# Optimization experiments

Measured on AMD Instinct MI355X. Metric: run time of the kernel, lower is better.

The kernel has to match this reference:

```python
import jax, jax.numpy as jnp
import numpy as np

D_OUT = 1536
BN_EPS = 1e-5


def _batchnorm(h, g, b):
    # torch BatchNorm1d in training mode: biased batch stats
    m = jnp.mean(h, axis=0)
    v = jnp.var(h, axis=0)
    return g * (h - m) * jax.lax.rsqrt(v + BN_EPS) + b


def setup_inputs() -> dict:
    key = jax.random.key(0)
    ks = jax.random.split(key, 16)
    B = 8192
    d0, d1, dib = 1024, 768, 1024
    s = lambda d: (2.0 / d) ** 0.5
    inp = {
        "x0": jax.random.normal(ks[0], (B, d0), jnp.float32),
        "x1": jax.random.normal(ks[1], (B, d1), jnp.float32),
        "x_ib": jax.random.normal(ks[2], (B, dib), jnp.float32),
        # 7 expert projections per source (Reaction_Head_mini modeled as linear proj)
        "pW0": jax.random.normal(ks[3], (7, d0, D_OUT), jnp.float32) * s(d0),
        "pb0": jnp.zeros((7, D_OUT), jnp.float32),
        "pW1": jax.random.normal(ks[4], (7, d1, D_OUT), jnp.float32) * s(d1),
        "pb1": jnp.zeros((7, D_OUT), jnp.float32),
        "pWib": jax.random.normal(ks[5], (7, dib, D_OUT), jnp.float32) * s(dib),
        "pbib": jnp.zeros((7, D_OUT), jnp.float32),
        # MOE_Router_Sig: Linear(1024,512)+BN+relu -> Linear(512,100)+BN+tanh -> Linear(100,3)
        "rw1": jax.random.normal(ks[6], (d0, 512), jnp.float32) * s(d0),
        "rb1": jnp.zeros((512,), jnp.float32),
        "rg1": jnp.ones((512,), jnp.float32),
        "rbt1": jnp.zeros((512,), jnp.float32),
        "rw2": jax.random.normal(ks[7], (512, 100), jnp.float32) * s(512),
        "rb2": jnp.zeros((100,), jnp.float32),
        "rg2": jnp.ones((100,), jnp.float32),
        "rbt2": jnp.zeros((100,), jnp.float32),
        "rw3": jax.random.normal(ks[8], (100, 3), jnp.float32) * s(100),
        "rb3": jnp.zeros((3,), jnp.float32),
    }
    return inp


def reference(x0, x1, x_ib, pW0, pb0, pW1, pb1, pWib, pbib,
              rw1, rb1, rg1, rbt1, rw2, rb2, rg2, rbt2, rw3, rb3):
    # ---- expert projections (torch.no_grad in original) ----
    e0 = jnp.einsum('bd,kdf->bkf', x0, pW0) + pb0      # [B,7,1536]
    e1 = jnp.einsum('bd,kdf->bkf', x1, pW1) + pb1      # [B,7,1536]
    eib = jnp.einsum('bd,kdf->bkf', x_ib, pWib) + pbib # [B,7,1536]
    ex = jnp.concatenate([e0, e1, eib], axis=1)        # [B,21,1536]
    B = ex.shape[0]
    # seg_mean with segment length 7 -> [B,3,1536]
    ex = ex.reshape(B, 3, 7, D_OUT).mean(axis=2)
    ex = jax.lax.stop_gradient(ex)
    # ---- router: MOE_Router_Sig(x0) -> sigmoid -> softmax ----
    h = _batchnorm(x0 @ rw1 + rb1, rg1, rbt1)
    h = jax.nn.relu(h)
    h = _batchnorm(h @ rw2 + rb2, rg2, rbt2)
    h = jnp.tanh(h)
    logits = jax.nn.sigmoid(h @ rw3 + rb3)             # [B,3]
    w = jax.nn.softmax(logits, axis=-1)                # [B,3]
    # ---- weighted combine + L2 normalize ----
    out = jnp.sum(ex * w[:, :, None], axis=1)          # [B,1536]
    out = out / jnp.linalg.norm(out, axis=-1, keepdims=True).clip(1e-12)
    return out
```

## Files before the change

kernel.cpp:

```cpp
#include <hip/hip_runtime.h>
#include <stdint.h>

typedef __attribute__((ext_vector_type(8))) short short8;
typedef __attribute__((ext_vector_type(4))) float floatx4;

__device__ inline unsigned short f2bf(float f) {
    unsigned int u = __float_as_uint(f);
    u += 0x7fffu + ((u >> 16) & 1u);
    return (unsigned short)(u >> 16);
}

__device__ void avg_transpose_tile(const float* __restrict__ src,
                                   unsigned short* __restrict__ dst,
                                   int E, int K, int Nsrc, int Ndst, int ldb,
                                   float scale, int tile_x, int tile_y) {
    __shared__ float tile[32][33];
    const int tid = threadIdx.x;
    const int tx = tid & 31;
    const int ty = tid >> 5;
    const int kb = tile_x * 32;
    const int nb = tile_y * 32;
#pragma unroll
    for (int p = 0; p < 4; ++p) {
        int kl = ty + p * 8;
        int k = kb + kl;
        int n = nb + tx;
        float s = 0.f;
        if (k < K && n < Nsrc) {
            for (int e = 0; e < E; ++e)
                s += src[(size_t)e * K * Nsrc + (size_t)k * Nsrc + n];
        }
        tile[kl][tx] = s * scale;
    }
    __syncthreads();
#pragma unroll
    for (int p = 0; p < 4; ++p) {
        int nl = ty + p * 8;
        int n = nb + nl;
        int k = kb + tx;
        if (n < Ndst && k < K)
            dst[(size_t)n * ldb + k] = f2bf(tile[tx][nl]);
    }
}

__global__ __launch_bounds__(256) void prep(
    const float* __restrict__ pW0, const float* __restrict__ pW1,
    const float* __restrict__ pWib, const float* __restrict__ rw1,
    const float* __restrict__ rw2, const float* __restrict__ pb0,
    const float* __restrict__ pb1, const float* __restrict__ pbib,
    const float* __restrict__ x0,
    unsigned short* __restrict__ Wmt, unsigned short* __restrict__ rw1t,
    unsigned short* __restrict__ rw2t, float* __restrict__ bm0,
    float* __restrict__ bm1, float* __restrict__ bm2,
    float* __restrict__ stats_zero, unsigned short* __restrict__ X0b) {
    int id = blockIdx.x;
    int tid = threadIdx.x;
    if (id < 1536) {
        avg_transpose_tile(pW0, Wmt + 0, 7, 1024, 1536, 1536, 2816, 1.f / 7.f,
                           id % 32, id / 32);
    } else if (id < 2688) {
        int t = id - 1536;
        avg_transpose_tile(pW1, Wmt + 1024, 7, 768, 1536, 1536, 2816, 1.f / 7.f,
                           t % 24, t / 24);
    } else if (id < 4224) {
        int t = id - 2688;
        avg_transpose_tile(pWib, Wmt + 1792, 7, 1024, 1536, 1536, 2816,
                           1.f / 7.f, t % 32, t / 32);
    } else if (id < 4736) {
        int t = id - 4224;
        avg_transpose_tile(rw1, rw1t, 1, 1024, 512, 512, 1024, 1.f, t % 32,
                           t / 32);
    } else if (id < 4800) {
        int t = id - 4736;
        avg_transpose_tile(rw2, rw2t, 1, 512, 100, 128, 512, 1.f, t % 16,
                           t / 16);
    } else if (id < 4806) {
        int i = (id - 4800) * 256 + tid;
        if (i < 1536) {
            float s0 = 0.f, s1 = 0.f, s2 = 0.f;
            for (int e = 0; e < 7; ++e) {
                s0 += pb0[e * 1536 + i];
                s1 += pb1[e * 1536 + i];
                s2 += pbib[e * 1536 + i];
            }
            const float inv = 1.f / 7.f;
            bm0[i] = s0 * inv; bm1[i] = s1 * inv; bm2[i] = s2 * inv;
        }
    } else if (id < 4807) {
        for (int i = tid; i < 1280; i += 256) stats_zero[i] = 0.f;
    } else {
        int base = (id - 4807) * 1024;
#pragma unroll
        for (int k = 0; k < 4; ++k) {
            int i = base + k * 256 + tid;
            float4 v = ((const float4*)x0)[i];
            ushort4 o;
            o.x = f2bf(v.x); o.y = f2bf(v.y); o.z = f2bf(v.z); o.w = f2bf(v.w);
            ((ushort4*)X0b)[i] = o;
        }
    }
}

template <int MODE>
__global__ __launch_bounds__(256) void gemm_bt(
    const unsigned short* __restrict__ A, const unsigned short* __restrict__ Bt,
    float* __restrict__ C, int K, int Nreal, int ldc,
    const float* __restrict__ bias, float* __restrict__ sum,
    float* __restrict__ sumsq) {
    __shared__ __align__(16) unsigned short As[128 * 32];
    __shared__ __align__(16) unsigned short Bs[128 * 32];
    const int tid = threadIdx.x;
    const int lane = tid & 63;
    const int wv = tid >> 6;
    const int bm_off = blockIdx.x * 128;
    const int bn_off = blockIdx.y * 128;
    const int wm = (wv & 1) * 64;
    const int wn = (wv >> 1) * 64;
    floatx4 acc[4][4];
#pragma unroll
    for (int i = 0; i < 4; ++i)
#pragma unroll
        for (int j = 0; j < 4; ++j) acc[i][j] = (floatx4){0.f, 0.f, 0.f, 0.f};

    const int quad = lane >> 4;
    const int lrow = lane & 15;
    const int srow = lane >> 2;
    const int scol = (lane & 3) * 8;

    const unsigned short* Ag = A + (size_t)bm_off * K;
    const unsigned short* Bg = Bt + (size_t)bn_off * K;

    for (int k0 = 0; k0 < K; k0 += 32) {
#pragma unroll
        for (int r = 0; r < 2; ++r) {
            int chunk = r * 4 + wv;
            {
                const unsigned short* gp =
                    Ag + (size_t)(chunk * 16 + srow) * K + (k0 + scol);
                __builtin_amdgcn_global_load_lds(
                    (const __attribute__((address_space(1))) void*)gp,
                    (__attribute__((address_space(3))) void*)(As + chunk * 512),
                    16, 0, 0);
            }
            {
                const unsigned short* gp =
                    Bg + (size_t)(chunk * 16 + srow) * K + (k0 + scol);
                __builtin_amdgcn_global_load_lds(
                    (const __attribute__((address_space(1))) void*)gp,
                    (__attribute__((address_space(3))) void*)(Bs + chunk * 512),
                    16, 0, 0);
            }
        }
        __syncthreads();
        short8 af[4], bfr[4];
#pragma unroll
        for (int i = 0; i < 4; ++i)
            af[i] = *(const short8*)(As + (wm + i * 16 + lrow) * 32 + quad * 8);
#pragma unroll
        for (int j = 0; j < 4; ++j)
            bfr[j] = *(const short8*)(Bs + (wn + j * 16 + lrow) * 32 + quad * 8);
#pragma unroll
        for (int i = 0; i < 4; ++i)
#pragma unroll
            for (int j = 0; j < 4; ++j)
                acc[i][j] = __builtin_amdgcn_mfma_f32_16x16x32_bf16(
                    af[i], bfr[j], acc[i][j], 0, 0, 0);
        __syncthreads();
    }

    {
#pragma unroll
        for (int j = 0; j < 4; ++j) {
            int n = bn_off + wn + j * 16 + lrow;
            bool nok = (n < Nreal);
            float bv = nok ? bias[n] : 0.f;
            float s = 0.f, ss = 0.f;
#pragma unroll
            for (int i = 0; i < 4; ++i) {
#pragma unroll
                for (int r = 0; r < 4; ++r) {
                    float v = acc[i][j][r] + bv;
                    int m = bm_off + wm + i * 16 + quad * 4 + r;
                    if (nok) C[(size_t)m * ldc + n] = v;
                    s += v; ss += v * v;
                }
            }
            s += __shfl_xor(s, 16); s += __shfl_xor(s, 32);
            ss += __shfl_xor(ss, 16); ss += __shfl_xor(ss, 32);
            if (quad == 0 && nok) {
                atomicAdd(&sum[n], s);
                atomicAdd(&sumsq[n], ss);
            }
        }
    }
}

__global__ __launch_bounds__(512, 2) void gemm256(
    const unsigned short* __restrict__ A0, const unsigned short* __restrict__ A1,
    const unsigned short* __restrict__ A2, const unsigned short* __restrict__ Bt,
    float* __restrict__ C, int ldc,
    const float* __restrict__ w0, const float* __restrict__ w1,
    const float* __restrict__ w2, const float* __restrict__ g0,
    const float* __restrict__ g1, const float* __restrict__ g2) {
    __shared__ __align__(16) unsigned short lds[57344];
    unsigned short* Asb = lds;
    unsigned short* Bsb = lds + 32768;

    const int tid = threadIdx.x;
    const int lane = tid & 63;
    const int wv = tid >> 6;
    const int wm = wv >> 2;
    const int wn = wv & 3;
    const int quad = lane >> 4;
    const int lrow = lane & 15;

    int b = blockIdx.y * 32 + blockIdx.x;
    const int xcd = b & 7;
    const int loc = b >> 3;
    const int row0 = (xcd * 4 + (loc & 3)) * 256;
    const int col0 = (loc >> 2) * 192;

    const int rA = tid >> 2;
    const int slA = (tid & 3) ^ ((rA >> 1) & 3);
    const size_t sA0 = (size_t)(row0 + rA) * 1024 + slA * 8;
    const size_t sA1 = (size_t)(row0 + rA) * 768 + slA * 8;

    size_t srcB16;
    {
        int r = tid >> 2;
        int sl = (tid & 3) ^ ((r >> 1) & 3);
        srcB16 = (size_t)(col0 + r) * 2816 + sl * 8;
    }
    size_t srcB4[2];
#pragma unroll
    for (int d = 0; d < 2; ++d) {
        int byteoff = d * 2048 + tid * 4;
        int r = 128 + (byteoff >> 6);
        int sl = ((byteoff >> 4) & 3) ^ ((r >> 1) & 3);
        srcB4[d] = (size_t)(col0 + r) * 2816 + sl * 8 + ((tid & 3) << 1);
    }

    auto stageA = [&](int kt, int buf) {
        unsigned short* d0 = Asb + buf * 8192 + wv * 512;
        if (kt < 32) {
            const unsigned short* g = A0 + (size_t)kt * 32;
            __builtin_amdgcn_global_load_lds(
                (const __attribute__((address_space(1))) void*)(g + sA0),
                (__attribute__((address_space(3))) void*)d0, 16, 0, 0);
            __builtin_amdgcn_global_load_lds(
                (const __attribute__((address_space(1))) void*)(g + sA0 + 128 * 1024),
                (__attribute__((address_space(3))) void*)(d0 + 4096), 16, 0, 0);
        } else if (kt < 56) {
            const unsigned short* g = A1 + (size_t)(kt - 32) * 32;
            __builtin_amdgcn_global_load_lds(
                (const __attribute__((address_space(1))) void*)(g + sA1),
                (__attribute__((address_space(3))) void*)d0, 16, 0, 0);
            __builtin_amdgcn_global_load_lds(
                (const __attribute__((address_space(1))) void*)(g + sA1 + 128 * 768),
                (__attribute__((address_space(3))) void*)(d0 + 4096), 16, 0, 0);
        } else {
            const unsigned short* g = A2 + (size_t)(kt - 56) * 32;
            __builtin_amdgcn_global_load_lds(
                (const __attribute__((address_space(1))) void*)(g + sA0),
                (__attribute__((address_space(3))) void*)d0, 16, 0, 0);
            __builtin_amdgcn_global_load_lds(
                (const __attribute__((address_space(1))) void*)(g + sA0 + 128 * 1024),
                (__attribute__((address_space(3))) void*)(d0 + 4096), 16, 0, 0);
        }
    };
    auto stageB = [&](int kt, int buf) {
        const size_t k0 = (size_t)kt * 32;
        __builtin_amdgcn_global_load_lds(
            (const __attribute__((address_space(1))) void*)(Bt + srcB16 + k0),
            (__attribute__((address_space(3))) void*)(Bsb + buf * 6144 +
                                                     wv * 512),
            16, 0, 0);
#pragma unroll
        for (int d = 0; d < 2; ++d) {
            __builtin_amdgcn_global_load_lds(
                (const __attribute__((address_space(1))) void*)(Bt + srcB4[d] + k0),
                (__attribute__((address_space(3))) void*)(Bsb + buf * 6144 +
                                                         4096 + d * 1024 +
                                                         wv * 128),
                4, 0, 0);
        }
    };

    floatx4 acc[8][3];
#pragma unroll
    for (int i = 0; i < 8; ++i)
#pragma unroll
        for (int j = 0; j < 3; ++j) acc[i][j] = (floatx4){0.f, 0.f, 0.f, 0.f};

    const int NT = 88;
    stageA(0, 0); stageB(0, 0);
    stageA(1, 1); stageB(1, 1);
    stageA(2, 2); stageB(2, 2);
    asm volatile("s_waitcnt vmcnt(10)" ::: "memory");
    asm volatile("s_barrier" ::: "memory");

    for (int t = 0; t < NT; ++t) {
        const int buf = t & 3;
        const int nb = (t + 3) & 3;
        const bool pre = (t + 3 < NT);
        const unsigned short* Ab = Asb + buf * 8192;
        const unsigned short* Bb = Bsb + buf * 6144;

        if (pre) stageA(t + 3, nb);
        short8 bfr[3];
#pragma unroll
        for (int j = 0; j < 3; ++j) {
            int r = wn * 48 + j * 16 + lrow;
            bfr[j] = *(const short8*)(Bb + r * 32 +
                                      ((quad ^ ((r >> 1) & 3)) << 3));
        }
        short8 af0[4];
#pragma unroll
        for (int i = 0; i < 4; ++i) {
            int r = wm * 128 + i * 16 + lrow;
            af0[i] = *(const short8*)(Ab + r * 32 +
                                      ((quad ^ ((r >> 1) & 3)) << 3));
        }
        __builtin_amdgcn_s_setprio(1);
#pragma unroll
        for (int i = 0; i < 4; ++i)
#pragma unroll
            for (int j = 0; j < 3; ++j)
                acc[i][j] = __builtin_amdgcn_mfma_f32_16x16x32_bf16(
                    af0[i], bfr[j], acc[i][j], 0, 0, 0);
        __builtin_amdgcn_s_setprio(0);

        if (pre) stageB(t + 3, nb);
        short8 af1[4];
#pragma unroll
        for (int i = 0; i < 4; ++i) {
            int r = wm * 128 + 64 + i * 16 + lrow;
            af1[i] = *(const short8*)(Ab + r * 32 +
                                      ((quad ^ ((r >> 1) & 3)) << 3));
        }
        __builtin_amdgcn_s_setprio(1);
#pragma unroll
        for (int i = 0; i < 4; ++i)
#pragma unroll
            for (int j = 0; j < 3; ++j)
                acc[4 + i][j] = __builtin_amdgcn_mfma_f32_16x16x32_bf16(
                    af1[i], bfr[j], acc[4 + i][j], 0, 0, 0);
        __builtin_amdgcn_s_setprio(0);

        if (t == 31) {
#pragma unroll
            for (int ii = 0; ii < 8; ++ii) {
#pragma unroll
                for (int r = 0; r < 4; ++r) {
                    float f = w0[row0 + wm * 128 + ii * 16 + quad * 4 + r];
#pragma unroll
                    for (int j = 0; j < 3; ++j) acc[ii][j][r] *= f;
                }
            }
        }

        if (t + 1 < NT) {
            if (t + 3 < NT)
                asm volatile("s_waitcnt vmcnt(10)" ::: "memory");
            else if (t + 2 < NT)
                asm volatile("s_waitcnt vmcnt(5)" ::: "memory");
            else
                asm volatile("s_waitcnt vmcnt(0)" ::: "memory");
            asm volatile("s_barrier" ::: "memory");
        }
    }

#pragma unroll
    for (int ii = 0; ii < 8; ++ii) {
#pragma unroll
        for (int r = 0; r < 4; ++r) {
            int m = row0 + wm * 128 + ii * 16 + quad * 4 + r;
            float a0 = w0[m], a1 = w1[m], a2 = w2[m];
#pragma unroll
            for (int j = 0; j < 3; ++j) {
                int n = col0 + wn * 48 + j * 16 + lrow;
                C[(size_t)m * ldc + n] =
                    acc[ii][j][r] + a0 * g0[n] + a1 * g1[n] + a2 * g2[n];
            }
        }
    }
}

__global__ __launch_bounds__(256) void bn_relu_pack(
    const float* __restrict__ h, unsigned short* __restrict__ out,
    const float* __restrict__ sum, const float* __restrict__ sumsq,
    const float* __restrict__ g, const float* __restrict__ b) {
    __shared__ float sc[512], sh[512];
    const float invB = 1.f / 8192.f;
    for (int c = threadIdx.x; c < 512; c += 256) {
        float m = sum[c] * invB;
        float v = sumsq[c] * invB - m * m;
        float s = g[c] * rsqrtf(v + 1e-5f);
        sc[c] = s;
        sh[c] = b[c] - m * s;
    }
    __syncthreads();
    int base = blockIdx.x * 4096;
#pragma unroll
    for (int k = 0; k < 16; ++k) {
        int i = base + k * 256 + threadIdx.x;
        int c4 = (i & 127) * 4;
        float4 v = ((const float4*)h)[i];
        ushort4 o;
        o.x = f2bf(fmaxf(v.x * sc[c4 + 0] + sh[c4 + 0], 0.f));
        o.y = f2bf(fmaxf(v.y * sc[c4 + 1] + sh[c4 + 1], 0.f));
        o.z = f2bf(fmaxf(v.z * sc[c4 + 2] + sh[c4 + 2], 0.f));
        o.w = f2bf(fmaxf(v.w * sc[c4 + 3] + sh[c4 + 3], 0.f));
        ((ushort4*)out)[i] = o;
    }
}

__global__ __launch_bounds__(128) void router_tail(
    const float* __restrict__ h2, const float* __restrict__ sum,
    const float* __restrict__ sumsq, const float* __restrict__ g,
    const float* __restrict__ b, const float* __restrict__ rw3,
    const float* __restrict__ rb3, float* __restrict__ w0,
    float* __restrict__ w1, float* __restrict__ w2) {
    __shared__ float sc[100], sh[100], w3[300], b3[3];
    int tid = threadIdx.x;
    const float invB = 1.f / 8192.f;
    if (tid < 100) {
        float m = sum[tid] * invB;
        float v = sumsq[tid] * invB - m * m;
        float s = g[tid] * rsqrtf(v + 1e-5f);
        sc[tid] = s;
        sh[tid] = b[tid] - m * s;
    }
    for (int i = tid; i < 300; i += 128) w3[i] = rw3[i];
    if (tid < 3) b3[tid] = rb3[tid];
    __syncthreads();
    int bi = blockIdx.x * 128 + tid;
    float l0 = b3[0], l1 = b3[1], l2 = b3[2];
    const float* hr = h2 + (size_t)bi * 100;
    for (int k = 0; k < 100; ++k) {
        float t = tanhf(hr[k] * sc[k] + sh[k]);
        l0 += t * w3[k * 3 + 0];
        l1 += t * w3[k * 3 + 1];
        l2 += t * w3[k * 3 + 2];
    }
    l0 = 1.f / (1.f + expf(-l0));
    l1 = 1.f / (1.f + expf(-l1));
    l2 = 1.f / (1.f + expf(-l2));
    float mx = fmaxf(l0, fmaxf(l1, l2));
    float e0 = expf(l0 - mx), e1 = expf(l1 - mx), e2 = expf(l2 - mx);
    float inv = 1.f / (e0 + e1 + e2);
    w0[bi] = e0 * inv; w1[bi] = e1 * inv; w2[bi] = e2 * inv;
}

__global__ __launch_bounds__(256) void pack1ib(
    const float* __restrict__ x1, const float* __restrict__ xib,
    const float* __restrict__ w1, const float* __restrict__ w2,
    unsigned short* __restrict__ X1b, unsigned short* __restrict__ Xib) {
    int i0 = blockIdx.x * 1024 + threadIdx.x;
#pragma unroll
    for (int k = 0; k < 4; ++k) {
        int i = i0 + k * 256;
        int b = i / 448;
        int g = i % 448;
        float w;
        const float* src;
        unsigned short* dst;
        if (g < 192) {
            w = w1[b];
            src = x1 + (size_t)b * 768 + g * 4;
            dst = X1b + (size_t)b * 768 + g * 4;
        } else {
            w = w2[b];
            src = xib + (size_t)b * 1024 + (g - 192) * 4;
            dst = Xib + (size_t)b * 1024 + (g - 192) * 4;
        }
        float4 v = *(const float4*)src;
        ushort4 o;
        o.x = f2bf(v.x * w); o.y = f2bf(v.y * w);
        o.z = f2bf(v.z * w); o.w = f2bf(v.w * w);
        *(ushort4*)dst = o;
    }
}

__global__ __launch_bounds__(256) void l2norm_rows(float* __restrict__ out) {
    int wv = threadIdx.x >> 6;
    int lane = threadIdx.x & 63;
    int row = blockIdx.x * 4 + wv;
    float4* rp = (float4*)(out + (size_t)row * 1536);
    float4 v[6];
    float ss = 0.f;
#pragma unroll
    for (int t = 0; t < 6; ++t) {
        v[t] = rp[lane + t * 64];
        ss += v[t].x * v[t].x + v[t].y * v[t].y + v[t].z * v[t].z + v[t].w * v[t].w;
    }
#pragma unroll
    for (int o = 32; o > 0; o >>= 1) ss += __shfl_xor(ss, o);
    float inv = 1.f / fmaxf(sqrtf(ss), 1e-12f);
#pragma unroll
    for (int t = 0; t < 6; ++t) {
        v[t].x *= inv; v[t].y *= inv; v[t].z *= inv; v[t].w *= inv;
        rp[lane + t * 64] = v[t];
    }
}

extern "C" void kernel_launch(void* const* d_in, const int* in_sizes, int n_in,
                              void* d_out, int out_size, void* d_ws,
                              size_t ws_size, hipStream_t stream) {
    (void)in_sizes; (void)n_in; (void)out_size; (void)ws_size;
    const float* x0   = (const float*)d_in[0];
    const float* x1   = (const float*)d_in[1];
    const float* xib  = (const float*)d_in[2];
    const float* pW0  = (const float*)d_in[3];
    const float* pb0  = (const float*)d_in[4];
    const float* pW1  = (const float*)d_in[5];
    const float* pb1  = (const float*)d_in[6];
    const float* pWib = (const float*)d_in[7];
    const float* pbib = (const float*)d_in[8];
    const float* rw1  = (const float*)d_in[9];
    const float* rb1  = (const float*)d_in[10];
    const float* rg1  = (const float*)d_in[11];
    const float* rbt1 = (const float*)d_in[12];
    const float* rw2  = (const float*)d_in[13];
    const float* rb2  = (const float*)d_in[14];
    const float* rg2  = (const float*)d_in[15];
    const float* rbt2 = (const float*)d_in[16];
    const float* rw3  = (const float*)d_in[17];
    const float* rb3  = (const float*)d_in[18];
    float* out = (float*)d_out;

    char* ws = (char*)d_ws;
    unsigned short* Wmt = (unsigned short*)(ws);
    char* stats = ws + 8650752;
    float* sum1   = (float*)(stats + 0);
    float* sumsq1 = (float*)(stats + 2048);
    float* sum2   = (float*)(stats + 4096);
    float* sumsq2 = (float*)(stats + 4608);
    float* bm0    = (float*)(stats + 10240);
    float* bm1    = (float*)(stats + 16384);
    float* bm2    = (float*)(stats + 22528);
    float* w0p    = (float*)(stats + 28672);
    float* w1p    = (float*)(stats + 61440);
    float* w2p    = (float*)(stats + 94208);
    unsigned short* rw1t = (unsigned short*)(ws + 8781824);
    unsigned short* rw2t = (unsigned short*)(ws + 9830400);
    char* R5 = ws + 9961472;
    unsigned short* X0b = (unsigned short*)(R5);
    float* h1           = (float*)(R5 + 16777216);
    unsigned short* h1n = (unsigned short*)(R5 + 33554432);
    float* h2           = (float*)(R5 + 41943040);
    unsigned short* X1b = (unsigned short*)(R5 + 16777216);
    unsigned short* Xib = (unsigned short*)(R5 + 29360128);

    prep<<<6855, 256, 0, stream>>>(pW0, pW1, pWib, rw1, rw2, pb0, pb1, pbib, x0,
                                   Wmt, rw1t, rw2t, bm0, bm1, bm2,
                                   (float*)stats, X0b);
    gemm_bt<2><<<dim3(64, 4), 256, 0, stream>>>(
        X0b, rw1t, h1, 1024, 512, 512, rb1, sum1, sumsq1);
    bn_relu_pack<<<256, 256, 0, stream>>>(h1, h1n, sum1, sumsq1, rg1, rbt1);
    gemm_bt<2><<<dim3(64, 1), 256, 0, stream>>>(
        h1n, rw2t, h2, 512, 100, 100, rb2, sum2, sumsq2);
    router_tail<<<64, 128, 0, stream>>>(h2, sum2, sumsq2, rg2, rbt2, rw3, rb3,
                                        w0p, w1p, w2p);
    pack1ib<<<3584, 256, 0, stream>>>(x1, xib, w1p, w2p, X1b, Xib);
    gemm256<<<dim3(32, 8), 512, 0, stream>>>(X0b, X1b, Xib, Wmt, out, 1536,
                                             w0p, w1p, w2p, bm0, bm1, bm2);
    l2norm_rows<<<2048, 256, 0, stream>>>(out);
}
```

Baseline: 416.7 us.

## Retile main GEMM to 256x256 tiles with BK=64 and ping-pong MFMA phases

Switches the fused expert GEMM from 256x192 tiles with K-step 32 to 256x256 tiles with K-step 64, so the grid drops from 256 to 192 blocks and each block does more MFMA work per staged tile. The B tile now loads with 16-byte async copies only, dropping the awkward 4-byte loads. The K-loop is split into four barrier-fenced MFMA phases with priority raising, interleaving the global-to-LDS prefetch between phases. It uses more LDS and accumulator registers, and 192 blocks may underfill a 256-CU device, which could hurt.

```diff
diff --git a/kernel.cpp b/kernel.cpp
--- a/kernel.cpp
+++ b/kernel.cpp
@@ -202,9 +202,7 @@
     const float* __restrict__ w0, const float* __restrict__ w1,
     const float* __restrict__ w2, const float* __restrict__ g0,
     const float* __restrict__ g1, const float* __restrict__ g2) {
-    __shared__ __align__(16) unsigned short lds[57344];
-    unsigned short* Asb = lds;
-    unsigned short* Bsb = lds + 32768;
+    __shared__ __align__(16) unsigned short lds[65536];
 
     const int tid = threadIdx.x;
     const int lane = tid & 63;
@@ -214,176 +212,181 @@
     const int quad = lane >> 4;
     const int lrow = lane & 15;
 
-    int b = blockIdx.y * 32 + blockIdx.x;
-    const int xcd = b & 7;
-    const int loc = b >> 3;
+    int id = blockIdx.y * 32 + blockIdx.x;
+    const int xcd = id & 7;
+    const int loc = id >> 3;
     const int row0 = (xcd * 4 + (loc & 3)) * 256;
-    const int col0 = (loc >> 2) * 192;
-
-    const int rA = tid >> 2;
-    const int slA = (tid & 3) ^ ((rA >> 1) & 3);
-    const size_t sA0 = (size_t)(row0 + rA) * 1024 + slA * 8;
-    const size_t sA1 = (size_t)(row0 + rA) * 768 + slA * 8;
-
-    size_t srcB16;
-    {
-        int r = tid >> 2;
-        int sl = (tid & 3) ^ ((r >> 1) & 3);
-        srcB16 = (size_t)(col0 + r) * 2816 + sl * 8;
-    }
-    size_t srcB4[2];
-#pragma unroll
-    for (int d = 0; d < 2; ++d) {
-        int byteoff = d * 2048 + tid * 4;
-        int r = 128 + (byteoff >> 6);
-        int sl = ((byteoff >> 4) & 3) ^ ((r >> 1) & 3);
-        srcB4[d] = (size_t)(col0 + r) * 2816 + sl * 8 + ((tid & 3) << 1);
-    }
-
-    auto stageA = [&](int kt, int buf) {
-        unsigned short* d0 = Asb + buf * 8192 + wv * 512;
-        if (kt < 32) {
-            const unsigned short* g = A0 + (size_t)kt * 32;
-            __builtin_amdgcn_global_load_lds(
-                (const __attribute__((address_space(1))) void*)(g + sA0),
-                (__attribute__((address_space(3))) void*)d0, 16, 0, 0);
-            __builtin_amdgcn_global_load_lds(
-                (const __attribute__((address_space(1))) void*)(g + sA0 + 128 * 1024),
-                (__attribute__((address_space(3))) void*)(d0 + 4096), 16, 0, 0);
-        } else if (kt < 56) {
-            const unsigned short* g = A1 + (size_t)(kt - 32) * 32;
-            __builtin_amdgcn_global_load_lds(
-                (const __attribute__((address_space(1))) void*)(g + sA1),
-                (__attribute__((address_space(3))) void*)d0, 16, 0, 0);
-            __builtin_amdgcn_global_load_lds(
-                (const __attribute__((address_space(1))) void*)(g + sA1 + 128 * 768),
-                (__attribute__((address_space(3))) void*)(d0 + 4096), 16, 0, 0);
-        } else {
-            const unsigned short* g = A2 + (size_t)(kt - 56) * 32;
-            __builtin_amdgcn_global_load_lds(
-                (const __attribute__((address_space(1))) void*)(g + sA0),
-                (__attribute__((address_space(3))) void*)d0, 16, 0, 0);
-            __builtin_amdgcn_global_load_lds(
-                (const __attribute__((address_space(1))) void*)(g + sA0 + 128 * 1024),
-                (__attribute__((address_space(3))) void*)(d0 + 4096), 16, 0, 0);
-        }
+    const int col0 = (loc >> 2) * 256;
+
+    const int rr = tid >> 3;
+    const int sl = (tid & 7) ^ (rr & 7);
+    const int sxor = lrow & 7;
+    const int brow = (wn & 1) * 64;
+
+    auto stA = [&](int kt, int mh) {
+        int slot = ((kt << 1) + mh) & 3;
+        const unsigned short* base;
+        int lda, koff;
+        if (kt < 16)      { base = A0; lda = 1024; koff = kt << 6; }
+        else if (kt < 28) { base = A1; lda = 768;  koff = (kt - 16) << 6; }
+        else              { base = A2; lda = 1024; koff = (kt - 28) << 6; }
+        const unsigned short* gp =
+            base + (size_t)(row0 + mh * 128 + rr) * lda + koff + sl * 8;
+        unsigned short* d = (unsigned short*)lds + slot * 8192 + wv * 512;
+        __builtin_amdgcn_global_load_lds(
+            (const __attribute__((address_space(1))) void*)gp,
+            (__attribute__((address_space(3))) void*)d, 16, 0, 0);
+        __builtin_amdgcn_global_load_lds(
+            (const __attribute__((address_space(1))) void*)(gp + (size_t)64 * lda),
+            (__attribute__((address_space(3))) void*)(d + 4096), 16, 0, 0);
     };
-    auto stageB = [&](int kt, int buf) {
-        const size_t k0 = (size_t)kt * 32;
+    auto stB = [&](int kt, int nh) {
+        int slot = ((kt << 1) + nh) & 3;
+        const unsigned short* gp =
+            Bt + (size_t)(col0 + nh * 128 + rr) * 2816 + (kt << 6) + sl * 8;
+        unsigned short* d = (unsigned short*)lds + 32768 + slot * 8192 + wv * 512;
         __builtin_amdgcn_global_load_lds(
-            (const __attribute__((address_space(1))) void*)(Bt + srcB16 + k0),
-            (__attribute__((address_space(3))) void*)(Bsb + buf * 6144 +
-                                                     wv * 512),
-            16, 0, 0);
-#pragma unroll
-        for (int d = 0; d < 2; ++d) {
-            __builtin_amdgcn_global_load_lds(
-                (const __attribute__((address_space(1))) void*)(Bt + srcB4[d] + k0),
-                (__attribute__((address_space(3))) void*)(Bsb + buf * 6144 +
-                                                         4096 + d * 1024 +
-                                                         wv * 128),
-                4, 0, 0);
-        }
+            (const __attribute__((address_space(1))) void*)gp,
+            (__attribute__((address_space(3))) void*)d, 16, 0, 0);
+        __builtin_amdgcn_global_load_lds(
+            (const __attribute__((address_space(1))) void*)(gp + (size_t)64 * 2816),
+            (__attribute__((address_space(3))) void*)(d + 4096), 16, 0, 0);
     };
 
-    floatx4 acc[8][3];
+#define LDA_FRAG(i, h) \
+    (*(const short8*)(Ar + ((i) * 16 + lrow) * 64 + ((((h) << 2) + quad) ^ sxor) * 8))
+#define LDB_FRAG(j, h) \
+    (*(const short8*)(Br + (brow + (j) * 16 + lrow) * 64 + ((((h) << 2) + quad) ^ sxor) * 8))
+#define MFMA_(d, a, b) \
+    d = __builtin_amdgcn_mfma_f32_16x16x32_bf16(a, b, d, 0, 0, 0)
+#define PRE_MFMA                                            \
+    asm volatile("s_barrier" ::: "memory");                 \
+    asm volatile("s_waitcnt lgkmcnt(0)" ::: "memory");      \
+    __builtin_amdgcn_sched_barrier(0);                      \
+    __builtin_amdgcn_s_setprio(1);
+#define POST_MFMA                                           \
+    __builtin_amdgcn_s_setprio(0);                          \
+    __builtin_amdgcn_sched_barrier(0);                      \
+    asm volatile("s_barrier" ::: "memory");
+
+    floatx4 acc[8][4];
 #pragma unroll
     for (int i = 0; i < 8; ++i)
 #pragma unroll
-        for (int j = 0; j < 3; ++j) acc[i][j] = (floatx4){0.f, 0.f, 0.f, 0.f};
-
-    const int NT = 88;
-    stageA(0, 0); stageB(0, 0);
-    stageA(1, 1); stageB(1, 1);
-    stageA(2, 2); stageB(2, 2);
-    asm volatile("s_waitcnt vmcnt(10)" ::: "memory");
+        for (int j = 0; j < 4; ++j) acc[i][j] = (floatx4){0.f, 0.f, 0.f, 0.f};
+
+    const int NT = 44;
+    stA(0, 0); stA(0, 1); stB(0, 0); stB(0, 1);
+    stA(1, 0); stA(1, 1); stB(1, 0); stB(1, 1);
+    asm volatile("s_waitcnt vmcnt(8)" ::: "memory");
     asm volatile("s_barrier" ::: "memory");
 
+    short8 af[4][2], bf0[2][2], bf1[2][2];
+#pragma unroll 2
     for (int t = 0; t < NT; ++t) {
-        const int buf = t & 3;
-        const int nb = (t + 3) & 3;
-        const bool pre = (t + 3 < NT);
-        const unsigned short* Ab = Asb + buf * 8192;
-        const unsigned short* Bb = Bsb + buf * 6144;
-
-        if (pre) stageA(t + 3, nb);
-        short8 bfr[3];
-#pragma unroll
-        for (int j = 0; j < 3; ++j) {
-            int r = wn * 48 + j * 16 + lrow;
-            bfr[j] = *(const short8*)(Bb + r * 32 +
-                                      ((quad ^ ((r >> 1) & 3)) << 3));
-        }
-        short8 af0[4];
+        const int pb = (t & 1) << 1;
+        const unsigned short* Ar = (const unsigned short*)lds + (pb + wm) * 8192;
+        const unsigned short* Br =
+            (const unsigned short*)lds + 32768 + (pb + (wn >> 1)) * 8192;
+
 #pragma unroll
         for (int i = 0; i < 4; ++i) {
-            int r = wm * 128 + i * 16 + lrow;
-            af0[i] = *(const short8*)(Ab + r * 32 +
-                                      ((quad ^ ((r >> 1) & 3)) << 3));
-        }
+            af[i][0] = LDA_FRAG(i, 0); af[i][1] = LDA_FRAG(i, 1);
+        }
+#pragma unroll
+        for (int j = 0; j < 2; ++j) {
+            bf0[j][0] = LDB_FRAG(j, 0); bf0[j][1] = LDB_FRAG(j, 1);
+        }
+        PRE_MFMA
+#pragma unroll
+        for (int h = 0; h < 2; ++h)
+#pragma unroll
+            for (int i = 0; i < 4; ++i)
+#pragma unroll
+                for (int j = 0; j < 2; ++j)
+                    MFMA_(acc[i][j], af[i][h], bf0[j][h]);
+        POST_MFMA
+
+#pragma unroll
+        for (int j = 0; j < 2; ++j) {
+            bf1[j][0] = LDB_FRAG(2 + j, 0); bf1[j][1] = LDB_FRAG(2 + j, 1);
+        }
+        PRE_MFMA
+#pragma unroll
+        for (int h = 0; h < 2; ++h)
+#pragma unroll
+            for (int i = 0; i < 4; ++i)
+#pragma unroll
+                for (int j = 0; j < 2; ++j)
+                    MFMA_(acc[i][2 + j], af[i][h], bf1[j][h]);
+        POST_MFMA
+
+#pragma unroll
+        for (int i = 0; i < 4; ++i) {
+            af[i][0] = LDA_FRAG(4 + i, 0); af[i][1] = LDA_FRAG(4 + i, 1);
+        }
+        if (t + 2 < NT) { stB(t + 2, 0); stB(t + 2, 1); }
+        PRE_MFMA
+#pragma unroll
+        for (int h = 0; h < 2; ++h)
+#pragma unroll
+            for (int i = 0; i < 4; ++i)
+#pragma unroll
+                for (int j = 0; j < 2; ++j)
+                    MFMA_(acc[4 + i][j], af[i][h], bf0[j][h]);
+        POST_MFMA
+
+        if (t + 2 < NT) { stA(t + 2, 0); stA(t + 2, 1); }
+        asm volatile("s_barrier" ::: "memory");
+        asm volatile("s_waitcnt lgkmcnt(0)" ::: "memory");
+        __builtin_amdgcn_sched_barrier(0);
         __builtin_amdgcn_s_setprio(1);
 #pragma unroll
-        for (int i = 0; i < 4; ++i)
-#pragma unroll
-            for (int j = 0; j < 3; ++j)
-                acc[i][j] = __builtin_amdgcn_mfma_f32_16x16x32_bf16(
-                    af0[i], bfr[j], acc[i][j], 0, 0, 0);
+        for (int h = 0; h < 2; ++h)
+#pragma unroll
+            for (int i = 0; i < 4; ++i)
+#pragma unroll
+                for (int j = 0; j < 2; ++j)
+                    MFMA_(acc[4 + i][2 + j], af[i][h], bf1[j][h]);
         __builtin_amdgcn_s_setprio(0);
-
-        if (pre) stageB(t + 3, nb);
-        short8 af1[4];
-#pragma unroll
-        for (int i = 0; i < 4; ++i) {
-            int r = wm * 128 + 64 + i * 16 + lrow;
-            af1[i] = *(const short8*)(Ab + r * 32 +
-                                      ((quad ^ ((r >> 1) & 3)) << 3));
-        }
-        __builtin_amdgcn_s_setprio(1);
-#pragma unroll
-        for (int i = 0; i < 4; ++i)
-#pragma unroll
-            for (int j = 0; j < 3; ++j)
-                acc[4 + i][j] = __builtin_amdgcn_mfma_f32_16x16x32_bf16(
-                    af1[i], bfr[j], acc[4 + i][j], 0, 0, 0);
-        __builtin_amdgcn_s_setprio(0);
-
-        if (t == 31) {
-#pragma unroll
-            for (int ii = 0; ii < 8; ++ii) {
+        __builtin_amdgcn_sched_barrier(0);
+        if (t < NT - 2)
+            asm volatile("s_waitcnt vmcnt(8)" ::: "memory");
+        else if (t == NT - 2)
+            asm volatile("s_waitcnt vmcnt(0)" ::: "memory");
+        asm volatile("s_barrier" ::: "memory");
+
+        if (t == 15) {
+#pragma unroll
+            for (int ii = 0; ii < 8; ++ii)
 #pragma unroll
                 for (int r = 0; r < 4; ++r) {
                     float f = w0[row0 + wm * 128 + ii * 16 + quad * 4 + r];
 #pragma unroll
-                    for (int j = 0; j < 3; ++j) acc[ii][j][r] *= f;
+                    for (int j = 0; j < 4; ++j) acc[ii][j][r] *= f;
                 }
+        }
+    }
+
+#pragma unroll
+    for (int i = 0; i < 8; ++i) {
+#pragma unroll
+        for (int r = 0; r < 4; ++r) {
+            int m = row0 + wm * 128 + i * 16 + quad * 4 + r;
+            float a0 = w0[m], a1 = w1[m], a2 = w2[m];
+#pragma unroll
+            for (int j = 0; j < 4; ++j) {
+                int n = col0 + wn * 64 + j * 16 + lrow;
+                C[(size_t)m * ldc + n] =
+                    acc[i][j][r] + a0 * g0[n] + a1 * g1[n] + a2 * g2[n];
             }
         }
-
-        if (t + 1 < NT) {
-            if (t + 3 < NT)
-                asm volatile("s_waitcnt vmcnt(10)" ::: "memory");
-            else if (t + 2 < NT)
-                asm volatile("s_waitcnt vmcnt(5)" ::: "memory");
-            else
-                asm volatile("s_waitcnt vmcnt(0)" ::: "memory");
-            asm volatile("s_barrier" ::: "memory");
-        }
-    }
-
-#pragma unroll
-    for (int ii = 0; ii < 8; ++ii) {
-#pragma unroll
-        for (int r = 0; r < 4; ++r) {
-            int m = row0 + wm * 128 + ii * 16 + quad * 4 + r;
-            float a0 = w0[m], a1 = w1[m], a2 = w2[m];
-#pragma unroll
-            for (int j = 0; j < 3; ++j) {
-                int n = col0 + wn * 48 + j * 16 + lrow;
-                C[(size_t)m * ldc + n] =
-                    acc[ii][j][r] + a0 * g0[n] + a1 * g1[n] + a2 * g2[n];
-            }
-        }
-    }
+    }
+#undef LDA_FRAG
+#undef LDB_FRAG
+#undef MFMA_
+#undef PRE_MFMA
+#undef POST_MFMA
 }
 
 __global__ __launch_bounds__(256) void bn_relu_pack(
@@ -563,7 +566,7 @@
     router_tail<<<64, 128, 0, stream>>>(h2, sum2, sumsq2, rg2, rbt2, rw3, rb3,
                                         w0p, w1p, w2p);
     pack1ib<<<3584, 256, 0, stream>>>(x1, xib, w1p, w2p, X1b, Xib);
-    gemm256<<<dim3(32, 8), 512, 0, stream>>>(X0b, X1b, Xib, Wmt, out, 1536,
+    gemm256<<<dim3(32, 6), 512, 0, stream>>>(X0b, X1b, Xib, Wmt, out, 1536,
                                              w0p, w1p, w2p, bm0, bm1, bm2);
     l2norm_rows<<<2048, 256, 0, stream>>>(out);
 }
```

Result: slower. 434.3 us (+4.2%).
